# Kernel optimization log

Hardware: AMD Instinct MI355X
Metric: run time of the kernel (lower is better)

The kernel has to match this reference:

```python
import jax, jax.numpy as jnp
import numpy as np
from jax import lax

B, NT, IN = 2048, 200, 128
LAT, NU, OU = 256, 512, 256
DHALF = IN // 2


def _mlp2(x, W1, b1, W2, b2):
    return jnp.tanh(x @ W1 + b1) @ W2 + b2


def setup_inputs() -> dict:
    key = jax.random.key(0)
    ks = jax.random.split(key, 16)
    w = lambda k, shp: jax.random.normal(k, shp, jnp.float32) * 0.05
    vals = jax.random.normal(ks[0], (B, NT, DHALF), jnp.float32)
    mask = (jax.random.uniform(ks[1], (B, NT, DHALF)) > 0.2).astype(jnp.float32)
    data = jnp.concatenate([vals * mask, mask], axis=-1)  # [B, NT, IN]
    time_steps = jnp.linspace(0.0, 1.0, NT).astype(jnp.float32)
    cat = 2 * LAT + IN
    return dict(
        data=data, time_steps=time_steps,
        Wu1=w(ks[2], (cat, NU)), bu1=jnp.zeros((NU,), jnp.float32),
        Wu2=w(ks[3], (NU, LAT)), bu2=jnp.zeros((LAT,), jnp.float32),
        Wr1=w(ks[4], (cat, NU)), br1=jnp.zeros((NU,), jnp.float32),
        Wr2=w(ks[5], (NU, LAT)), br2=jnp.zeros((LAT,), jnp.float32),
        Wn1=w(ks[6], (cat, NU)), bn1=jnp.zeros((NU,), jnp.float32),
        Wn2=w(ks[7], (NU, 2 * LAT)), bn2=jnp.zeros((2 * LAT,), jnp.float32),
        Wo1=w(ks[8], (LAT, OU)), bo1=jnp.zeros((OU,), jnp.float32),
        Wo2=w(ks[9], (OU, LAT)), bo2=jnp.zeros((LAT,), jnp.float32),
        Wt1=w(ks[10], (2 * LAT, 100)), bt1=jnp.zeros((100,), jnp.float32),
        Wt2=w(ks[11], (100, 2 * LAT)), bt2=jnp.zeros((2 * LAT,), jnp.float32),
    )


def reference(data, time_steps, Wu1, bu1, Wu2, bu2, Wr1, br1, Wr2, br2,
              Wn1, bn1, Wn2, bn2, Wo1, bo1, Wo2, bo2, Wt1, bt1, Wt2, bt2):
    # run_backwards=True: iterate timesteps from last to first.
    xs = data.transpose(1, 0, 2)[::-1]  # [NT, B, IN]
    # Euler dt per iteration: first is t[-1]-(t[-1]+0.01)=-0.01, then t[i]-t[i+1].
    dts = jnp.concatenate([jnp.array([-0.01], jnp.float32),
                           (time_steps[:-1] - time_steps[1:])[::-1]])

    def step(carry, xt):
        y, s = carry
        x, dt = xt
        # Euler ODE evolve (gap always < minimum_step for uniform grid)
        y_ode = y + _mlp2(y, Wo1, bo1, Wo2, bo2) * dt
        yc = jnp.concatenate([y_ode, s, x], axis=-1)  # [B, 2*LAT+IN]
        u = jax.nn.sigmoid(_mlp2(yc, Wu1, bu1, Wu2, bu2))
        r = jax.nn.sigmoid(_mlp2(yc, Wr1, br1, Wr2, br2))
        c2 = jnp.concatenate([y_ode * r, s * r, x], axis=-1)
        ns = _mlp2(c2, Wn1, bn1, Wn2, bn2)
        new_state = ns[..., :LAT]
        new_std = jnp.abs(ns[..., LAT:])
        ny = (1.0 - u) * new_state + u * y_ode
        nstd = (1.0 - u) * new_std + u * s
        m = (jnp.sum(x[..., DHALF:], axis=-1, keepdims=True) > 0).astype(y.dtype)
        ny = m * ny + (1.0 - m) * y_ode
        nstd = jnp.abs(m * nstd + (1.0 - m) * s)
        return (ny, nstd), None

    init = (jnp.zeros((B, LAT), data.dtype), jnp.zeros((B, LAT), data.dtype))
    (last_y, last_std), _ = lax.scan(step, init, (xs, dts))

    z = _mlp2(jnp.concatenate([last_y, last_std], axis=-1), Wt1, bt1, Wt2, bt2)
    mean_z0 = z[..., :LAT]
    std_z0 = jnp.clip(jnp.abs(z[..., LAT:]), 1e-20)
    return mean_z0[None], std_z0[None]  # [1, B, LAT] each
```

## Files before the change

### kernel.cpp

```cpp
#include <hip/hip_runtime.h>
#include <hip/hip_bf16.h>

#define B_TOT 2048
#define NTS   200
#define DIN   128
#define LATN  256
#define ROWS  16
#define NBLK  (B_TOT/ROWS)
#define NTHR  1024

#define CATP  648
#define HURP  1032

#define OFF_WO1   0
#define OFF_WO2   65536
#define OFF_WUR1  131072
#define OFF_WUR2  786432
#define OFF_WN1   1048576
#define OFF_WN2   1376256
#define WS_ELEMS  1638400

typedef __attribute__((ext_vector_type(8))) short s8v;
typedef __attribute__((ext_vector_type(4))) float f4v;

__device__ __forceinline__ unsigned short f2bf(float x) {
    __hip_bfloat16 h = __float2bfloat16(x);
    unsigned short u;
    __builtin_memcpy(&u, &h, 2);
    return u;
}

__device__ __forceinline__ float fast_tanh(float x) {
    float e = __expf(2.f * x);
    return 1.f - 2.f * __builtin_amdgcn_rcpf(e + 1.f);
}
__device__ __forceinline__ float fast_sig(float x) {
    return __builtin_amdgcn_rcpf(1.f + __expf(-x));
}

template<int K, int NFR>
__device__ __forceinline__ void mmloop(const unsigned short* A, int strideA,
                                       const unsigned short* bp, int rot,
                                       f4v* acc, int arow, int ah)
{
    constexpr int NS = K / 32;
    const unsigned short* ap = A + arow * strideA + ah * 8;
    s8v bcur[NFR], bnxt[NFR];
    s8v acur, anxt;
    int c = rot;
    acur = *(const s8v*)(ap + c * 32);
#pragma unroll
    for (int f = 0; f < NFR; ++f) bcur[f] = *(const s8v*)(bp + f * NS * 512 + c * 512);
#pragma unroll 2
    for (int s = 0; s < NS; ++s) {
        int cn = c + 1; if (cn >= NS) cn = 0;
        if (s + 1 < NS) {
            anxt = *(const s8v*)(ap + cn * 32);
#pragma unroll
            for (int f = 0; f < NFR; ++f)
                bnxt[f] = *(const s8v*)(bp + f * NS * 512 + cn * 512);
        }
#pragma unroll
        for (int f = 0; f < NFR; ++f)
            acc[f] = __builtin_amdgcn_mfma_f32_16x16x32_bf16(acur, bcur[f], acc[f], 0, 0, 0);
        if (s + 1 < NS) {
            acur = anxt;
#pragma unroll
            for (int f = 0; f < NFR; ++f) bcur[f] = bnxt[f];
        }
        c = cn;
    }
}

__device__ __forceinline__ void tile_decode(int e, int K, int& col, int& k) {
    const int NS = K / 32;
    int cb  = e / (NS * 512);
    int rem = e - cb * (NS * 512);
    int s   = rem >> 9;
    int q   = rem & 511;
    int l   = q >> 3;
    int j   = q & 7;
    col = cb * 16 + (l & 15);
    k   = s * 32 + (l >> 4) * 8 + j;
}

__global__ void prep_weights(const float* __restrict__ Wu1, const float* __restrict__ Wr1,
                             const float* __restrict__ Wu2, const float* __restrict__ Wr2,
                             const float* __restrict__ Wn1, const float* __restrict__ Wn2,
                             const float* __restrict__ Wo1, const float* __restrict__ Wo2,
                             unsigned short* __restrict__ ws)
{
    int idx = blockIdx.x * 256 + threadIdx.x;
    if (idx >= WS_ELEMS) return;
    float v;
    int col, k;
    if (idx < OFF_WO2) {
        tile_decode(idx - OFF_WO1, 256, col, k);
        v = Wo1[k * 256 + col];
    } else if (idx < OFF_WUR1) {
        tile_decode(idx - OFF_WO2, 256, col, k);
        v = Wo2[k * 256 + col];
    } else if (idx < OFF_WUR2) {
        tile_decode(idx - OFF_WUR1, 640, col, k);
        v = (col < 512) ? Wu1[k * 512 + col] : Wr1[k * 512 + (col - 512)];
    } else if (idx < OFF_WN1) {
        tile_decode(idx - OFF_WUR2, 512, col, k);
        v = (col < 256) ? Wu2[k * 256 + col] : Wr2[k * 256 + (col - 256)];
    } else if (idx < OFF_WN2) {
        tile_decode(idx - OFF_WN1, 640, col, k);
        v = Wn1[k * 512 + col];
    } else {
        tile_decode(idx - OFF_WN2, 512, col, k);
        v = Wn2[k * 512 + col];
    }
    ws[idx] = f2bf(v);
}

__launch_bounds__(NTHR)
__global__ void odernn_main(const float* __restrict__ data, const float* __restrict__ tsg,
                            const float* __restrict__ bu1, const float* __restrict__ bu2,
                            const float* __restrict__ br1, const float* __restrict__ br2,
                            const float* __restrict__ bn1, const float* __restrict__ bn2,
                            const float* __restrict__ bo1, const float* __restrict__ bo2,
                            const float* __restrict__ Wt1, const float* __restrict__ bt1,
                            const float* __restrict__ Wt2, const float* __restrict__ bt2,
                            const unsigned short* __restrict__ W,
                            float* __restrict__ out)
{
    __shared__ unsigned short cat[ROWS][CATP];
    __shared__ unsigned short hur[ROWS][HURP];
    __shared__ float yf [ROWS][LATN];
    __shared__ float sf [ROWS][LATN];
    __shared__ float yof[ROWS][LATN];
    __shared__ float uf [ROWS][LATN];
    __shared__ float z1s[ROWS][100];
    __shared__ float msum[2][ROWS];
    __shared__ float bL[3072];

    const int tid  = threadIdx.x;
    const int lane = tid & 63;
    const int w    = tid >> 6;
    const int arow = lane & 15;
    const int ah   = lane >> 4;
    const int r0   = blockIdx.x * ROWS;
    const int rot  = (blockIdx.x >> 3) & 15;
    const int rot8 = rot & 7;

    for (int i = tid; i < ROWS * LATN; i += NTHR) {
        yf[i >> 8][i & 255] = 0.f;
        sf[i >> 8][i & 255] = 0.f;
    }
    for (int i = tid; i < ROWS * 512; i += NTHR)
        cat[i >> 9][i & 511] = 0;
    for (int i = tid; i < 3072; i += NTHR) {
        float v;
        if      (i <  256) v = bo1[i];
        else if (i <  512) v = bo2[i - 256];
        else if (i < 1024) v = bu1[i - 512];
        else if (i < 1536) v = br1[i - 1024];
        else if (i < 1792) v = bu2[i - 1536];
        else if (i < 2048) v = br2[i - 1792];
        else if (i < 2560) v = bn1[i - 2048];
        else               v = bn2[i - 2560];
        bL[i] = v;
    }
    const int xc = lane * 2;
    {
        const float2 xv = *(const float2*)(data + ((size_t)(r0 + w) * NTS + 199) * DIN + xc);
        cat[w][512 + xc + 0] = f2bf(xv.x);
        cat[w][512 + xc + 1] = f2bf(xv.y);
        float mp = (xc >= 64) ? (xv.x + xv.y) : 0.f;
#pragma unroll
        for (int m = 32; m >= 1; m >>= 1) mp += __shfl_xor(mp, m, 64);
        if (lane == 0) msum[0][w] = mp;
    }
    __syncthreads();

    for (int t = 0; t < NTS; ++t) {
        const float dtv = (t == 0) ? -0.01f : (tsg[199 - t] - tsg[200 - t]);

        {
            f4v a[1];
            float b = bL[w * 16 + arow];
            a[0] = (f4v){b, b, b, b};
            mmloop<256, 1>(&cat[0][0], CATP, W + OFF_WO1 + w * 8 * 512 + lane * 8, rot8, a, arow, ah);
#pragma unroll
            for (int i = 0; i < 4; ++i) {
                int row = ah * 4 + i, col = w * 16 + arow;
                hur[row][col] = f2bf(fast_tanh(a[0][i]));
            }
        }
        __syncthreads();

        {
            f4v a[1];
            float b = bL[256 + w * 16 + arow];
            a[0] = (f4v){b, b, b, b};
            mmloop<256, 1>(&hur[0][0], HURP, W + OFF_WO2 + w * 8 * 512 + lane * 8, rot8, a, arow, ah);
#pragma unroll
            for (int i = 0; i < 4; ++i) {
                int row = ah * 4 + i, col = w * 16 + arow;
                float yo = yf[row][col] + a[0][i] * dtv;
                yof[row][col] = yo;
                cat[row][col] = f2bf(yo);
            }
        }
        __syncthreads();

#pragma unroll 1
        for (int p = 0; p < 2; ++p) {
            f4v a[2];
#pragma unroll
            for (int f = 0; f < 2; ++f) {
                float b = bL[512 + w * 64 + p * 32 + f * 16 + arow];
                a[f] = (f4v){b, b, b, b};
            }
            mmloop<640, 2>(&cat[0][0], CATP,
                           W + OFF_WUR1 + (w * 4 + p * 2) * 20 * 512 + lane * 8, rot, a, arow, ah);
#pragma unroll
            for (int f = 0; f < 2; ++f)
#pragma unroll
                for (int i = 0; i < 4; ++i) {
                    int row = ah * 4 + i, col = w * 64 + p * 32 + f * 16 + arow;
                    hur[row][col] = f2bf(fast_tanh(a[f][i]));
                }
        }
        __syncthreads();

        {
            f4v a[2];
            const int c0 = w * 32;
#pragma unroll
            for (int f = 0; f < 2; ++f) {
                float b = bL[1536 + c0 + f * 16 + arow];
                a[f] = (f4v){b, b, b, b};
            }
            const int aoff = (w < 8) ? 0 : 512;
            mmloop<512, 2>(&hur[0][0] + aoff, HURP, W + OFF_WUR2 + (w * 2) * 16 * 512 + lane * 8, rot, a, arow, ah);
#pragma unroll
            for (int f = 0; f < 2; ++f)
#pragma unroll
                for (int i = 0; i < 4; ++i) {
                    int row = ah * 4 + i, j = c0 + f * 16 + arow;
                    float sg = fast_sig(a[f][i]);
                    if (j < 256) {
                        uf[row][j] = sg;
                    } else {
                        int c = j - 256;
                        float yo = yof[row][c], so = sf[row][c];
                        cat[row][c]       = f2bf(yo * sg);
                        cat[row][256 + c] = f2bf(so * sg);
                    }
                }
        }
        __syncthreads();

        float2 xv;
        const bool hasx = (t + 1 < NTS);
        if (hasx)
            xv = *(const float2*)(data + ((size_t)(r0 + w) * NTS + (198 - t)) * DIN + xc);
        {
            f4v a[2];
#pragma unroll
            for (int f = 0; f < 2; ++f) {
                float b = bL[2048 + w * 32 + f * 16 + arow];
                a[f] = (f4v){b, b, b, b};
            }
            mmloop<640, 2>(&cat[0][0], CATP, W + OFF_WN1 + (w * 2) * 20 * 512 + lane * 8, rot, a, arow, ah);
#pragma unroll
            for (int f = 0; f < 2; ++f)
#pragma unroll
                for (int i = 0; i < 4; ++i) {
                    int row = ah * 4 + i, col = w * 32 + f * 16 + arow;
                    hur[row][col] = f2bf(fast_tanh(a[f][i]));
                }
        }
        __syncthreads();

        {
            f4v a[2];
#pragma unroll
            for (int f = 0; f < 2; ++f) {
                float b = bL[2560 + w * 32 + f * 16 + arow];
                a[f] = (f4v){b, b, b, b};
            }
            mmloop<512, 2>(&hur[0][0], HURP, W + OFF_WN2 + (w * 2) * 16 * 512 + lane * 8, rot, a, arow, ah);
#pragma unroll
            for (int f = 0; f < 2; ++f)
#pragma unroll
                for (int i = 0; i < 4; ++i) {
                    int row = ah * 4 + i, j = w * 32 + f * 16 + arow;
                    float val = a[f][i];
                    bool m = msum[t & 1][row] > 0.f;
                    if (j < 256) {
                        float u  = uf[row][j];
                        float yo = yof[row][j];
                        float ny = (1.f - u) * val + u * yo;
                        float yn = m ? ny : yo;
                        yf[row][j] = yn;
                        cat[row][j] = f2bf(yn);
                    } else {
                        int c = j - 256;
                        float u  = uf[row][c];
                        float so = sf[row][c];
                        float nstd = (1.f - u) * fabsf(val) + u * so;
                        float sn = m ? nstd : so;
                        sn = fabsf(sn);
                        sf[row][c] = sn;
                        cat[row][256 + c] = f2bf(sn);
                    }
                }
        }
        if (hasx) {
            cat[w][512 + xc + 0] = f2bf(xv.x);
            cat[w][512 + xc + 1] = f2bf(xv.y);
            float mp = (xc >= 64) ? (xv.x + xv.y) : 0.f;
#pragma unroll
            for (int m = 32; m >= 1; m >>= 1) mp += __shfl_xor(mp, m, 64);
            if (lane == 0) msum[(t + 1) & 1][w] = mp;
        }
        __syncthreads();
    }

    for (int it = tid; it < ROWS * 100; it += NTHR) {
        int r = it / 100, j = it - r * 100;
        float acc = bt1[j];
        for (int k = 0; k < 256; ++k) acc += yf[r][k] * Wt1[k * 100 + j];
        for (int k = 0; k < 256; ++k) acc += sf[r][k] * Wt1[(256 + k) * 100 + j];
        z1s[r][j] = fast_tanh(acc);
    }
    __syncthreads();
    for (int it = tid; it < ROWS * 512; it += NTHR) {
        int r = it >> 9, j = it & 511;
        float acc = bt2[j];
        for (int k = 0; k < 100; ++k) acc += z1s[r][k] * Wt2[k * 512 + j];
        int bg = r0 + r;
        if (j < 256) {
            out[(size_t)bg * 256 + j] = acc;
        } else {
            float v = fabsf(acc);
            if (v < 1e-20f) v = 1e-20f;
            out[(size_t)B_TOT * 256 + (size_t)bg * 256 + (j - 256)] = v;
        }
    }
}

extern "C" void kernel_launch(void* const* d_in, const int* in_sizes, int n_in,
                              void* d_out, int out_size, void* d_ws, size_t ws_size,
                              hipStream_t stream) {
    const float* data = (const float*)d_in[0];
    const float* ts   = (const float*)d_in[1];
    const float* Wu1  = (const float*)d_in[2];
    const float* bu1  = (const float*)d_in[3];
    const float* Wu2  = (const float*)d_in[4];
    const float* bu2  = (const float*)d_in[5];
    const float* Wr1  = (const float*)d_in[6];
    const float* br1  = (const float*)d_in[7];
    const float* Wr2  = (const float*)d_in[8];
    const float* br2  = (const float*)d_in[9];
    const float* Wn1  = (const float*)d_in[10];
    const float* bn1  = (const float*)d_in[11];
    const float* Wn2  = (const float*)d_in[12];
    const float* bn2  = (const float*)d_in[13];
    const float* Wo1  = (const float*)d_in[14];
    const float* bo1  = (const float*)d_in[15];
    const float* Wo2  = (const float*)d_in[16];
    const float* bo2  = (const float*)d_in[17];
    const float* Wt1  = (const float*)d_in[18];
    const float* bt1  = (const float*)d_in[19];
    const float* Wt2  = (const float*)d_in[20];
    const float* bt2  = (const float*)d_in[21];
    unsigned short* ws = (unsigned short*)d_ws;
    float* out = (float*)d_out;

    prep_weights<<<(WS_ELEMS + 255) / 256, 256, 0, stream>>>(
        Wu1, Wr1, Wu2, Wr2, Wn1, Wn2, Wo1, Wo2, ws);
    odernn_main<<<NBLK, NTHR, 0, stream>>>(
        data, ts, bu1, bu2, br1, br2, bn1, bn2, bo1, bo2,
        Wt1, bt1, Wt2, bt2, ws, out);
}
```

Measured before the change: 5.409 ms.

## Quantize ODE and update/reset weights to per-column scaled FP8, others to FP16

Stores the Wo1/Wo2 and Wu/Wr weight matrices as FP8 with per-output-column scales, decoded in registers to FP16 before running FP16 MFMAs. The Wn weights and all activations switch from BF16 to FP16. The goal is to halve the weight bytes streamed from L2/HBM in every one of the 200 timesteps, since the recurrent loop is dominated by weight loads. In exchange it adds per-element decode ALU work inside the inner loop and a scale-plus-bias epilogue, and it carries an accuracy risk from FP8 weights and the narrower FP16 range.

```diff
diff --git a/kernel.cpp b/kernel.cpp
--- a/kernel.cpp
+++ b/kernel.cpp
@@ -12,19 +12,21 @@
 #define CATP  648
 #define HURP  1032
 
-#define OFF_WO1   0
-#define OFF_WO2   65536
-#define OFF_WUR1  131072
-#define OFF_WUR2  786432
-#define OFF_WN1   1048576
-#define OFF_WN2   1376256
-#define WS_ELEMS  1638400
-
-typedef __attribute__((ext_vector_type(8))) short s8v;
-typedef __attribute__((ext_vector_type(4))) float f4v;
-
-__device__ __forceinline__ unsigned short f2bf(float x) {
-    __hip_bfloat16 h = __float2bfloat16(x);
+#define OFF8_O1   0
+#define OFF8_O2   65536
+#define OFF8_UR1  131072
+#define OFF8_UR2  786432
+#define OFF16_N1  1048576
+#define OFF16_N2  1703936
+#define OFF_SC    2228224
+
+typedef __attribute__((ext_vector_type(8))) _Float16 h8v;
+typedef __attribute__((ext_vector_type(2))) __fp16   q2v;
+typedef __attribute__((ext_vector_type(2))) float    f2v;
+typedef __attribute__((ext_vector_type(4))) float    f4v;
+
+__device__ __forceinline__ unsigned short f2h(float x) {
+    _Float16 h = (_Float16)x;
     unsigned short u;
     __builtin_memcpy(&u, &h, 2);
     return u;
@@ -38,31 +40,46 @@
     return __builtin_amdgcn_rcpf(1.f + __expf(-x));
 }
 
+__device__ __forceinline__ h8v dec8(uint2 b) {
+    f2v p0 = __builtin_amdgcn_cvt_pk_f32_fp8(b.x, false);
+    f2v p1 = __builtin_amdgcn_cvt_pk_f32_fp8(b.x, true);
+    f2v p2 = __builtin_amdgcn_cvt_pk_f32_fp8(b.y, false);
+    f2v p3 = __builtin_amdgcn_cvt_pk_f32_fp8(b.y, true);
+    union { h8v h; q2v q[4]; } u;
+    u.q[0] = __builtin_amdgcn_cvt_pkrtz(p0.x, p0.y);
+    u.q[1] = __builtin_amdgcn_cvt_pkrtz(p1.x, p1.y);
+    u.q[2] = __builtin_amdgcn_cvt_pkrtz(p2.x, p2.y);
+    u.q[3] = __builtin_amdgcn_cvt_pkrtz(p3.x, p3.y);
+    return u.h;
+}
+
 template<int K, int NFR>
-__device__ __forceinline__ void mmloop(const unsigned short* A, int strideA,
-                                       const unsigned short* bp, int rot,
-                                       f4v* acc, int arow, int ah)
+__device__ __forceinline__ void mmloop8(const unsigned short* A, int strideA,
+                                        const unsigned char* bp, int rot,
+                                        f4v* acc, int arow, int ah)
 {
     constexpr int NS = K / 32;
     const unsigned short* ap = A + arow * strideA + ah * 8;
-    s8v bcur[NFR], bnxt[NFR];
-    s8v acur, anxt;
+    uint2 bcur[NFR], bnxt[NFR];
+    h8v acur, anxt;
     int c = rot;
-    acur = *(const s8v*)(ap + c * 32);
-#pragma unroll
-    for (int f = 0; f < NFR; ++f) bcur[f] = *(const s8v*)(bp + f * NS * 512 + c * 512);
+    acur = *(const h8v*)(ap + c * 32);
+#pragma unroll
+    for (int f = 0; f < NFR; ++f) bcur[f] = *(const uint2*)(bp + f * NS * 512 + c * 512);
 #pragma unroll 2
     for (int s = 0; s < NS; ++s) {
         int cn = c + 1; if (cn >= NS) cn = 0;
         if (s + 1 < NS) {
-            anxt = *(const s8v*)(ap + cn * 32);
+            anxt = *(const h8v*)(ap + cn * 32);
 #pragma unroll
             for (int f = 0; f < NFR; ++f)
-                bnxt[f] = *(const s8v*)(bp + f * NS * 512 + cn * 512);
-        }
-#pragma unroll
-        for (int f = 0; f < NFR; ++f)
-            acc[f] = __builtin_amdgcn_mfma_f32_16x16x32_bf16(acur, bcur[f], acc[f], 0, 0, 0);
+                bnxt[f] = *(const uint2*)(bp + f * NS * 512 + cn * 512);
+        }
+#pragma unroll
+        for (int f = 0; f < NFR; ++f) {
+            h8v bh = dec8(bcur[f]);
+            acc[f] = __builtin_amdgcn_mfma_f32_16x16x32_f16(acur, bh, acc[f], 0, 0, 0);
+        }
         if (s + 1 < NS) {
             acur = anxt;
 #pragma unroll
@@ -70,6 +87,72 @@
         }
         c = cn;
     }
+}
+
+template<int K, int NFR>
+__device__ __forceinline__ void mmloop16(const unsigned short* A, int strideA,
+                                         const unsigned short* bp16, int rot,
+                                         f4v* acc, int arow, int ah)
+{
+    constexpr int NS = K / 32;
+    const unsigned short* ap = A + arow * strideA + ah * 8;
+    h8v bcur[NFR], bnxt[NFR];
+    h8v acur, anxt;
+    int c = rot;
+    acur = *(const h8v*)(ap + c * 32);
+#pragma unroll
+    for (int f = 0; f < NFR; ++f) bcur[f] = *(const h8v*)(bp16 + f * NS * 512 + c * 512);
+#pragma unroll 2
+    for (int s = 0; s < NS; ++s) {
+        int cn = c + 1; if (cn >= NS) cn = 0;
+        if (s + 1 < NS) {
+            anxt = *(const h8v*)(ap + cn * 32);
+#pragma unroll
+            for (int f = 0; f < NFR; ++f)
+                bnxt[f] = *(const h8v*)(bp16 + f * NS * 512 + cn * 512);
+        }
+#pragma unroll
+        for (int f = 0; f < NFR; ++f)
+            acc[f] = __builtin_amdgcn_mfma_f32_16x16x32_f16(acur, bcur[f], acc[f], 0, 0, 0);
+        if (s + 1 < NS) {
+            acur = anxt;
+#pragma unroll
+            for (int f = 0; f < NFR; ++f) bcur[f] = bnxt[f];
+        }
+        c = cn;
+    }
+}
+
+__global__ void prep_fp8(const float* __restrict__ Wo1, const float* __restrict__ Wo2,
+                         const float* __restrict__ Wu1, const float* __restrict__ Wr1,
+                         const float* __restrict__ Wu2, const float* __restrict__ Wr2,
+                         unsigned char* __restrict__ ws8, float* __restrict__ scg)
+{
+    int gwid = (blockIdx.x * blockDim.x + threadIdx.x) >> 6;
+    int lane = threadIdx.x & 63;
+    if (gwid >= 2048) return;
+    const float* src; int K, N, scol, off8, scb, col;
+    if (gwid < 256)       { col = gwid;        K = 256; N = 256; src = Wo1; scol = col; off8 = OFF8_O1;  scb = 0; }
+    else if (gwid < 512)  { col = gwid - 256;  K = 256; N = 256; src = Wo2; scol = col; off8 = OFF8_O2;  scb = 256; }
+    else if (gwid < 1536) { col = gwid - 512;  K = 640; N = 512; src = (col < 512) ? Wu1 : Wr1; scol = col & 511; off8 = OFF8_UR1; scb = 512; }
+    else                  { col = gwid - 1536; K = 512; N = 256; src = (col < 256) ? Wu2 : Wr2; scol = col & 255; off8 = OFF8_UR2; scb = 1536; }
+    float amax = 0.f;
+    for (int k = lane; k < K; k += 64)
+        amax = fmaxf(amax, fabsf(src[k * N + scol]));
+#pragma unroll
+    for (int m = 32; m >= 1; m >>= 1)
+        amax = fmaxf(amax, __shfl_xor(amax, m, 64));
+    const float inv = (amax > 0.f) ? 240.f / amax : 0.f;
+    const int NS = K / 32;
+    const int cb = col >> 4, lcol = col & 15;
+    for (int k = lane; k < K; k += 64) {
+        float v = src[k * N + scol] * inv;
+        unsigned byte = (unsigned)__builtin_amdgcn_cvt_pk_fp8_f32(v, v, 0, false) & 0xffu;
+        int s = k >> 5, kk = k & 31;
+        int l8 = ((kk >> 3) << 4) | lcol;
+        ws8[off8 + cb * (NS * 512) + s * 512 + l8 * 8 + (kk & 7)] = (unsigned char)byte;
+    }
+    if (lane == 0) scg[scb + col] = (amax > 0.f) ? amax / 240.f : 0.f;
 }
 
 __device__ __forceinline__ void tile_decode(int e, int K, int& col, int& k) {
@@ -84,36 +167,20 @@
     k   = s * 32 + (l >> 4) * 8 + j;
 }
 
-__global__ void prep_weights(const float* __restrict__ Wu1, const float* __restrict__ Wr1,
-                             const float* __restrict__ Wu2, const float* __restrict__ Wr2,
-                             const float* __restrict__ Wn1, const float* __restrict__ Wn2,
-                             const float* __restrict__ Wo1, const float* __restrict__ Wo2,
-                             unsigned short* __restrict__ ws)
+__global__ void prep_n16(const float* __restrict__ Wn1, const float* __restrict__ Wn2,
+                         unsigned short* __restrict__ ws16)
 {
-    int idx = blockIdx.x * 256 + threadIdx.x;
-    if (idx >= WS_ELEMS) return;
-    float v;
+    int e = blockIdx.x * 256 + threadIdx.x;
+    if (e >= 589824) return;
     int col, k;
-    if (idx < OFF_WO2) {
-        tile_decode(idx - OFF_WO1, 256, col, k);
-        v = Wo1[k * 256 + col];
-    } else if (idx < OFF_WUR1) {
-        tile_decode(idx - OFF_WO2, 256, col, k);
-        v = Wo2[k * 256 + col];
-    } else if (idx < OFF_WUR2) {
-        tile_decode(idx - OFF_WUR1, 640, col, k);
-        v = (col < 512) ? Wu1[k * 512 + col] : Wr1[k * 512 + (col - 512)];
-    } else if (idx < OFF_WN1) {
-        tile_decode(idx - OFF_WUR2, 512, col, k);
-        v = (col < 256) ? Wu2[k * 256 + col] : Wr2[k * 256 + (col - 256)];
-    } else if (idx < OFF_WN2) {
-        tile_decode(idx - OFF_WN1, 640, col, k);
-        v = Wn1[k * 512 + col];
+    if (e < 327680) {
+        tile_decode(e, 640, col, k);
+        ws16[e] = f2h(Wn1[k * 512 + col]);
     } else {
-        tile_decode(idx - OFF_WN2, 512, col, k);
-        v = Wn2[k * 512 + col];
-    }
-    ws[idx] = f2bf(v);
+        int e2 = e - 327680;
+        tile_decode(e2, 512, col, k);
+        ws16[e] = f2h(Wn2[k * 512 + col]);
+    }
 }
 
 __launch_bounds__(NTHR)
@@ -124,7 +191,7 @@
                             const float* __restrict__ bo1, const float* __restrict__ bo2,
                             const float* __restrict__ Wt1, const float* __restrict__ bt1,
                             const float* __restrict__ Wt2, const float* __restrict__ bt2,
-                            const unsigned short* __restrict__ W,
+                            const unsigned char* __restrict__ Wb,
                             float* __restrict__ out)
 {
     __shared__ unsigned short cat[ROWS][CATP];
@@ -136,6 +203,11 @@
     __shared__ float z1s[ROWS][100];
     __shared__ float msum[2][ROWS];
     __shared__ float bL[3072];
+    __shared__ float scL[2048];
+
+    const unsigned short* W16n1 = (const unsigned short*)(Wb + OFF16_N1);
+    const unsigned short* W16n2 = (const unsigned short*)(Wb + OFF16_N2);
+    const float* scg = (const float*)(Wb + OFF_SC);
 
     const int tid  = threadIdx.x;
     const int lane = tid & 63;
@@ -164,11 +236,13 @@
         else               v = bn2[i - 2560];
         bL[i] = v;
     }
+    for (int i = tid; i < 2048; i += NTHR)
+        scL[i] = scg[i];
     const int xc = lane * 2;
     {
         const float2 xv = *(const float2*)(data + ((size_t)(r0 + w) * NTS + 199) * DIN + xc);
-        cat[w][512 + xc + 0] = f2bf(xv.x);
-        cat[w][512 + xc + 1] = f2bf(xv.y);
+        cat[w][512 + xc + 0] = f2h(xv.x);
+        cat[w][512 + xc + 1] = f2h(xv.y);
         float mp = (xc >= 64) ? (xv.x + xv.y) : 0.f;
 #pragma unroll
         for (int m = 32; m >= 1; m >>= 1) mp += __shfl_xor(mp, m, 64);
@@ -180,78 +254,73 @@
         const float dtv = (t == 0) ? -0.01f : (tsg[199 - t] - tsg[200 - t]);
 
         {
-            f4v a[1];
-            float b = bL[w * 16 + arow];
-            a[0] = (f4v){b, b, b, b};
-            mmloop<256, 1>(&cat[0][0], CATP, W + OFF_WO1 + w * 8 * 512 + lane * 8, rot8, a, arow, ah);
+            f4v a[1] = {{0.f, 0.f, 0.f, 0.f}};
+            mmloop8<256, 1>(&cat[0][0], CATP, Wb + OFF8_O1 + w * 8 * 512 + lane * 8, rot8, a, arow, ah);
+            const float sc = scL[w * 16 + arow], b = bL[w * 16 + arow];
 #pragma unroll
             for (int i = 0; i < 4; ++i) {
                 int row = ah * 4 + i, col = w * 16 + arow;
-                hur[row][col] = f2bf(fast_tanh(a[0][i]));
+                hur[row][col] = f2h(fast_tanh(a[0][i] * sc + b));
             }
         }
         __syncthreads();
 
         {
-            f4v a[1];
-            float b = bL[256 + w * 16 + arow];
-            a[0] = (f4v){b, b, b, b};
-            mmloop<256, 1>(&hur[0][0], HURP, W + OFF_WO2 + w * 8 * 512 + lane * 8, rot8, a, arow, ah);
+            f4v a[1] = {{0.f, 0.f, 0.f, 0.f}};
+            mmloop8<256, 1>(&hur[0][0], HURP, Wb + OFF8_O2 + w * 8 * 512 + lane * 8, rot8, a, arow, ah);
+            const float sc = scL[256 + w * 16 + arow], b = bL[256 + w * 16 + arow];
 #pragma unroll
             for (int i = 0; i < 4; ++i) {
                 int row = ah * 4 + i, col = w * 16 + arow;
-                float yo = yf[row][col] + a[0][i] * dtv;
+                float yo = yf[row][col] + (a[0][i] * sc + b) * dtv;
                 yof[row][col] = yo;
-                cat[row][col] = f2bf(yo);
+                cat[row][col] = f2h(yo);
             }
         }
         __syncthreads();
 
 #pragma unroll 1
         for (int p = 0; p < 2; ++p) {
-            f4v a[2];
+            f4v a[2] = {{0.f, 0.f, 0.f, 0.f}, {0.f, 0.f, 0.f, 0.f}};
+            mmloop8<640, 2>(&cat[0][0], CATP,
+                            Wb + OFF8_UR1 + (w * 4 + p * 2) * 20 * 512 + lane * 8, rot, a, arow, ah);
 #pragma unroll
             for (int f = 0; f < 2; ++f) {
-                float b = bL[512 + w * 64 + p * 32 + f * 16 + arow];
-                a[f] = (f4v){b, b, b, b};
-            }
-            mmloop<640, 2>(&cat[0][0], CATP,
-                           W + OFF_WUR1 + (w * 4 + p * 2) * 20 * 512 + lane * 8, rot, a, arow, ah);
-#pragma unroll
-            for (int f = 0; f < 2; ++f)
+                int col = w * 64 + p * 32 + f * 16 + arow;
+                const float sc = scL[512 + col], b = bL[512 + col];
 #pragma unroll
                 for (int i = 0; i < 4; ++i) {
-                    int row = ah * 4 + i, col = w * 64 + p * 32 + f * 16 + arow;
-                    hur[row][col] = f2bf(fast_tanh(a[f][i]));
+                    int row = ah * 4 + i;
+                    hur[row][col] = f2h(fast_tanh(a[f][i] * sc + b));
                 }
+            }
         }
         __syncthreads();
 
         {
-            f4v a[2];
+            f4v a[2] = {{0.f, 0.f, 0.f, 0.f}, {0.f, 0.f, 0.f, 0.f}};
             const int c0 = w * 32;
+            const int aoff = (w < 8) ? 0 : 512;
+            mmloop8<512, 2>(&hur[0][0] + aoff, HURP,
+                            Wb + OFF8_UR2 + (w * 2) * 16 * 512 + lane * 8, rot, a, arow, ah);
 #pragma unroll
             for (int f = 0; f < 2; ++f) {
-                float b = bL[1536 + c0 + f * 16 + arow];
-                a[f] = (f4v){b, b, b, b};
-            }
-            const int aoff = (w < 8) ? 0 : 512;
-            mmloop<512, 2>(&hur[0][0] + aoff, HURP, W + OFF_WUR2 + (w * 2) * 16 * 512 + lane * 8, rot, a, arow, ah);
-#pragma unroll
-            for (int f = 0; f < 2; ++f)
+                int j = c0 + f * 16 + arow;
+                const float sc = scL[1536 + j], b = bL[1536 + j];
 #pragma unroll
                 for (int i = 0; i < 4; ++i) {
-                    int row = ah * 4 + i, j = c0 + f * 16 + arow;
-                    float sg = fast_sig(a[f][i]);
+                    int row = ah * 4 + i;
+                    float sg = fast_sig(a[f][i] * sc + b);
                     if (j < 256) {
                         uf[row][j] = sg;
                     } else {
                         int c = j - 256;
                         float yo = yof[row][c], so = sf[row][c];
-                        cat[row][c]       = f2bf(yo * sg);
-                        cat[row][256 + c] = f2bf(so * sg);
+                        cat[row][c]       = f2h(yo * sg);
+                        cat[row][256 + c] = f2h(so * sg);
                     }
                 }
+            }
         }
         __syncthreads();
 
@@ -266,13 +335,13 @@
                 float b = bL[2048 + w * 32 + f * 16 + arow];
                 a[f] = (f4v){b, b, b, b};
             }
-            mmloop<640, 2>(&cat[0][0], CATP, W + OFF_WN1 + (w * 2) * 20 * 512 + lane * 8, rot, a, arow, ah);
+            mmloop16<640, 2>(&cat[0][0], CATP, W16n1 + (w * 2) * 20 * 512 + lane * 8, rot, a, arow, ah);
 #pragma unroll
             for (int f = 0; f < 2; ++f)
 #pragma unroll
                 for (int i = 0; i < 4; ++i) {
                     int row = ah * 4 + i, col = w * 32 + f * 16 + arow;
-                    hur[row][col] = f2bf(fast_tanh(a[f][i]));
+                    hur[row][col] = f2h(fast_tanh(a[f][i]));
                 }
         }
         __syncthreads();
@@ -284,7 +353,7 @@
                 float b = bL[2560 + w * 32 + f * 16 + arow];
                 a[f] = (f4v){b, b, b, b};
             }
-            mmloop<512, 2>(&hur[0][0], HURP, W + OFF_WN2 + (w * 2) * 16 * 512 + lane * 8, rot, a, arow, ah);
+            mmloop16<512, 2>(&hur[0][0], HURP, W16n2 + (w * 2) * 16 * 512 + lane * 8, rot, a, arow, ah);
 #pragma unroll
             for (int f = 0; f < 2; ++f)
 #pragma unroll
@@ -298,7 +367,7 @@
                         float ny = (1.f - u) * val + u * yo;
                         float yn = m ? ny : yo;
                         yf[row][j] = yn;
-                        cat[row][j] = f2bf(yn);
+                        cat[row][j] = f2h(yn);
                     } else {
                         int c = j - 256;
                         float u  = uf[row][c];
@@ -307,13 +376,13 @@
                         float sn = m ? nstd : so;
                         sn = fabsf(sn);
                         sf[row][c] = sn;
-                        cat[row][256 + c] = f2bf(sn);
+                        cat[row][256 + c] = f2h(sn);
                     }
                 }
         }
         if (hasx) {
-            cat[w][512 + xc + 0] = f2bf(xv.x);
-            cat[w][512 + xc + 1] = f2bf(xv.y);
+            cat[w][512 + xc + 0] = f2h(xv.x);
+            cat[w][512 + xc + 1] = f2h(xv.y);
             float mp = (xc >= 64) ? (xv.x + xv.y) : 0.f;
 #pragma unroll
             for (int m = 32; m >= 1; m >>= 1) mp += __shfl_xor(mp, m, 64);
@@ -370,12 +439,14 @@
     const float* bt1  = (const float*)d_in[19];
     const float* Wt2  = (const float*)d_in[20];
     const float* bt2  = (const float*)d_in[21];
-    unsigned short* ws = (unsigned short*)d_ws;
+    unsigned char* ws8 = (unsigned char*)d_ws;
+    float* scg = (float*)(ws8 + OFF_SC);
+    unsigned short* ws16 = (unsigned short*)(ws8 + OFF16_N1);
     float* out = (float*)d_out;
 
-    prep_weights<<<(WS_ELEMS + 255) / 256, 256, 0, stream>>>(
-        Wu1, Wr1, Wu2, Wr2, Wn1, Wn2, Wo1, Wo2, ws);
+    prep_fp8<<<512, 256, 0, stream>>>(Wo1, Wo2, Wu1, Wr1, Wu2, Wr2, ws8, scg);
+    prep_n16<<<2304, 256, 0, stream>>>(Wn1, Wn2, ws16);
     odernn_main<<<NBLK, NTHR, 0, stream>>>(
         data, ts, bu1, bu2, br1, br2, bn1, bn2, bo1, bo2,
-        Wt1, bt1, Wt2, bt2, ws, out);
-}
+        Wt1, bt1, Wt2, bt2, ws8, out);
+}
```

Result: slower. 5.543 ms (+2.5%).
